# Kernel tuning notes

Hardware: AMD Instinct MI355X
Metric: run time of the kernel (lower is better)

## Reference

```python
import jax, jax.numpy as jnp
import numpy as np
import math

HEAD_DIM = 128
N_HEADS = 32
N_KV_HEADS = 8
ROPE_THETA = 10000.0


def _rotate_half(x):
    x1, x2 = jnp.split(x, 2, axis=-1)
    return jnp.concatenate([-x2, x1], axis=-1)


def _rope_cos_sin(position_ids, head_dim, theta):
    # position_ids: [B, S] int
    inv_freq = 1.0 / (theta ** (jnp.arange(0, head_dim, 2, dtype=jnp.float32) / head_dim))
    freqs = position_ids.astype(jnp.float32)[..., None] * inv_freq[None, None, :]  # [B,S,D/2]
    emb = jnp.concatenate([freqs, freqs], axis=-1)  # [B,S,D]
    return jnp.cos(emb), jnp.sin(emb)


def setup_inputs() -> dict:
    key = jax.random.key(0)
    k1, k2, k3, k4, k5 = jax.random.split(key, 5)
    B, S, H = 1, 2048, 4096
    hidden_states = jax.random.normal(k1, (B, S, H), dtype=jnp.float32)
    Wq = jax.random.normal(k2, (N_HEADS * HEAD_DIM, H), dtype=jnp.float32) * (1.0 / math.sqrt(H))
    Wk = jax.random.normal(k3, (N_KV_HEADS * HEAD_DIM, H), dtype=jnp.float32) * (1.0 / math.sqrt(H))
    Wv = jax.random.normal(k4, (N_KV_HEADS * HEAD_DIM, H), dtype=jnp.float32) * (1.0 / math.sqrt(H))
    Wo = jax.random.normal(k5, (H, N_HEADS * HEAD_DIM), dtype=jnp.float32) * (1.0 / math.sqrt(H))
    position_ids = jnp.arange(S, dtype=jnp.int32)[None, :]
    return {"hidden_states": hidden_states, "Wq": Wq, "Wk": Wk, "Wv": Wv, "Wo": Wo,
            "position_ids": position_ids}


def reference(hidden_states, Wq, Wk, Wv, Wo, position_ids):
    B, S, H = hidden_states.shape
    d = HEAD_DIM
    groups = N_HEADS // N_KV_HEADS

    # projections (torch Linear: x @ W^T)
    q = (hidden_states @ Wq.T).reshape(B, S, N_HEADS, d).transpose(0, 2, 1, 3)      # [B,Hq,S,d]
    k = (hidden_states @ Wk.T).reshape(B, S, N_KV_HEADS, d).transpose(0, 2, 1, 3)   # [B,Hk,S,d]
    v = (hidden_states @ Wv.T).reshape(B, S, N_KV_HEADS, d).transpose(0, 2, 1, 3)

    cos, sin = _rope_cos_sin(position_ids, d, ROPE_THETA)  # [B,S,d]
    cos = cos[:, None, :, :]
    sin = sin[:, None, :, :]
    q = q * cos + _rotate_half(q) * sin
    k = k * cos + _rotate_half(k) * sin

    # GQA: repeat kv heads
    k = jnp.repeat(k, groups, axis=1)  # [B,Hq,S,d]
    v = jnp.repeat(v, groups, axis=1)

    scores = jnp.einsum('bhqd,bhkd->bhqk', q, k) / math.sqrt(d)
    causal = jnp.tril(jnp.ones((S, S), dtype=bool))
    scores = jnp.where(causal[None, None], scores, jnp.finfo(jnp.float32).min)
    attn = jax.nn.softmax(scores.astype(jnp.float32), axis=-1).astype(q.dtype)

    out = jnp.einsum('bhqk,bhkd->bhqd', attn, v)        # [B,Hq,S,d]
    out = out.transpose(0, 2, 1, 3).reshape(B, S, N_HEADS * d)
    return out @ Wo.T
```

## Files before the change

### kernel.cpp

```cpp
#include <hip/hip_runtime.h>
#include <hip/hip_bf16.h>
#include <cstdint>
#include <cstddef>

#define S_LEN 2048
#define HID   4096
#define HD    128
#define NH    32
#define NKV   8
#define KVW   (NKV * HD)
#define QKVN  (HID + 2 * KVW)

typedef __bf16 bf16x8_t __attribute__((ext_vector_type(8)));
typedef float  f32x4_t  __attribute__((ext_vector_type(4)));
typedef unsigned short u16x8_t __attribute__((ext_vector_type(8)));

__device__ __forceinline__ unsigned short f2b(float f) {
  unsigned u = __float_as_uint(f);
  u += 0x7FFFu + ((u >> 16) & 1u);
  return (unsigned short)(u >> 16);
}
__device__ __forceinline__ float b2f(unsigned short v) {
  return __uint_as_float(((unsigned)v) << 16);
}
__device__ __forceinline__ void gld_lds16(const void* g, void* l) {
  __builtin_amdgcn_global_load_lds(
      (const __attribute__((address_space(1))) void*)g,
      (__attribute__((address_space(3))) void*)l, 16, 0, 0);
}

__global__ void cvt_kernel(const float* __restrict__ src,
                           unsigned short* __restrict__ dst, int n4) {
  int i = blockIdx.x * blockDim.x + threadIdx.x;
  int stride = gridDim.x * blockDim.x;
  for (; i < n4; i += stride) {
    float4 v = reinterpret_cast<const float4*>(src)[i];
    ushort4 o;
    o.x = f2b(v.x); o.y = f2b(v.y); o.z = f2b(v.z); o.w = f2b(v.w);
    reinterpret_cast<ushort4*>(dst)[i] = o;
  }
}

__global__ void rope_kernel(unsigned short* __restrict__ Q,
                            unsigned short* __restrict__ Kb,
                            const int* __restrict__ pos_ids) {
  const int total = S_LEN * (NH + NKV) * 64;
  int idx = blockIdx.x * blockDim.x + threadIdx.x;
  int stride = gridDim.x * blockDim.x;
  for (; idx < total; idx += stride) {
    int s   = idx / ((NH + NKV) * 64);
    int rem = idx % ((NH + NKV) * 64);
    int hp  = rem >> 6;
    int i   = rem & 63;
    unsigned short* ptr; int W, h;
    if (hp < NH) { ptr = Q;  W = HID; h = hp; }
    else         { ptr = Kb; W = KVW; h = hp - NH; }
    float pos = (float)pos_ids[s];
    float ang = pos * __expf(-(float)i * 0.14391156516f);
    float sn, cs;
    sincosf(ang, &sn, &cs);
    size_t base = (size_t)s * W + (size_t)h * HD + i;
    float lo = b2f(ptr[base]);
    float hi = b2f(ptr[base + 64]);
    ptr[base]      = f2b(lo * cs - hi * sn);
    ptr[base + 64] = f2b(hi * cs + lo * sn);
  }
}

template <int BN, int MODE>
__global__ __launch_bounds__(512, 4) void gemm4p_kernel(
    const unsigned short* __restrict__ A, const unsigned short* __restrict__ B,
    void* __restrict__ C0, void* __restrict__ C1, void* __restrict__ C2,
    int N, int K) {
  constexpr int NFR = BN / 64;
  constexpr int ABYTES = 128 * 128;
  constexpr int TILE_LDS = ABYTES + BN * 128;
  __shared__ char ldsB[2 * TILE_LDS];

  const int tid  = threadIdx.x;
  const int lane = tid & 63;
  const int wid  = tid >> 6;
  const int wm = wid >> 2, wn = wid & 3;
  const int lr = lane & 15, g = lane >> 4;
  const int bm = blockIdx.y * 128;
  const int bn = blockIdx.x * BN;
  const int nk = K >> 6;
  const int ni = nk >> 1;
  const int xr = (lr & 7) << 4;

  auto stage_u = [&](int t, int u) {
    if (t >= nk) return;
    const int riu = tid >> 3;
    const int cbs = ((tid & 7) << 4) ^ ((riu & 7) << 4);
    const char* src;
    if (u < 2)
      src = (const char*)A + ((size_t)(bm + u * 64 + riu) * K + t * 64) * 2 + cbs;
    else
      src = (const char*)B + ((size_t)(bn + (u - 2) * 64 + riu) * K + t * 64) * 2 + cbs;
    gld_lds16(src, ldsB + (t & 1) * TILE_LDS + u * 8192 + tid * 16);
  };

  auto rdA = [&](const char* bb, int m, int k) {
    const int row = wm * 64 + m * 16 + lr;
    return *(const bf16x8_t*)(bb + row * 128 + ((k * 64 + g * 16) ^ xr));
  };
  auto rdB = [&](const char* bb, int n, int k) {
    const int row = wn * (BN / 4) + n * 16 + lr;
    return *(const bf16x8_t*)(bb + ABYTES + row * 128 + ((k * 64 + g * 16) ^ xr));
  };

  for (int t = 0; t < 2; ++t)
    for (int u = 0; u < 2 + NFR; ++u) stage_u(t, u);
  asm volatile("s_waitcnt vmcnt(0)" ::: "memory");
  __builtin_amdgcn_sched_barrier(0);
  __builtin_amdgcn_s_barrier();

  f32x4_t acc[4][NFR];
#pragma unroll
  for (int m = 0; m < 4; ++m)
#pragma unroll
    for (int n = 0; n < NFR; ++n) acc[m][n] = f32x4_t{0.f, 0.f, 0.f, 0.f};

  bf16x8_t bfr[NFR][2], af[2][2];

#define MFMA_BLOCK(MB)                                                        \
  __builtin_amdgcn_s_setprio(1);                                              \
  _Pragma("unroll") for (int m = 0; m < 2; ++m)                               \
    _Pragma("unroll") for (int n = 0; n < NFR; ++n)                           \
      _Pragma("unroll") for (int k = 0; k < 2; ++k)                           \
        acc[(MB) + m][n] = __builtin_amdgcn_mfma_f32_16x16x32_bf16(           \
            af[m][k], bfr[n][k], acc[(MB) + m][n], 0, 0, 0);                  \
  __builtin_amdgcn_s_setprio(0);

#define GATE()                                                                \
  __builtin_amdgcn_s_barrier();                                               \
  asm volatile("s_waitcnt lgkmcnt(0)" ::: "memory");                          \
  __builtin_amdgcn_sched_barrier(0);

#define RD_A2(bb, m0)                                                         \
  _Pragma("unroll") for (int m = 0; m < 2; ++m)                               \
    _Pragma("unroll") for (int k = 0; k < 2; ++k)                             \
      af[m][k] = rdA(bb, (m0) + m, k);

#define RD_B(bb)                                                              \
  _Pragma("unroll") for (int n = 0; n < NFR; ++n)                             \
    _Pragma("unroll") for (int k = 0; k < 2; ++k)                             \
      bfr[n][k] = rdB(bb, n, k);

  for (int i = 0; i < ni; ++i) {
    const char* bE = ldsB;
    const char* bO = ldsB + TILE_LDS;
    const int tO = 2 * i + 1, tE2 = 2 * i + 2, tO2 = 2 * i + 3;
    const bool last = (i == ni - 1);

    RD_B(bE);
    RD_A2(bE, 0);
    if (i > 0) { stage_u(tO, 0); stage_u(tO, 1); }
    GATE(); MFMA_BLOCK(0);
    __builtin_amdgcn_s_barrier();

    RD_A2(bE, 2);
#pragma unroll
    for (int u = 0; u < NFR; ++u) stage_u(tE2, 2 + u);
    GATE(); MFMA_BLOCK(2);
    if (last) { asm volatile("s_waitcnt vmcnt(0)" ::: "memory"); }
    else      { asm volatile("s_waitcnt vmcnt(%0)" :: "n"(NFR) : "memory"); }
    __builtin_amdgcn_sched_barrier(0);
    __builtin_amdgcn_s_barrier();

    RD_B(bO);
    RD_A2(bO, 0);
    stage_u(tE2, 0); stage_u(tE2, 1);
    GATE(); MFMA_BLOCK(0);
    __builtin_amdgcn_s_barrier();

    RD_A2(bO, 2);
#pragma unroll
    for (int u = 0; u < NFR; ++u) stage_u(tO2, 2 + u);
    GATE(); MFMA_BLOCK(2);
    if (!last) { asm volatile("s_waitcnt vmcnt(%0)" :: "n"(NFR) : "memory"); }
    __builtin_amdgcn_sched_barrier(0);
    __builtin_amdgcn_s_barrier();
  }
#undef MFMA_BLOCK
#undef GATE
#undef RD_A2
#undef RD_B

#pragma unroll
  for (int mf = 0; mf < 4; ++mf) {
    const int row0 = bm + wm * 64 + mf * 16 + g * 4;
#pragma unroll
    for (int nf = 0; nf < NFR; ++nf) {
      const int col = bn + wn * (BN / 4) + nf * 16 + lr;
      if constexpr (MODE == 1) {
#pragma unroll
        for (int r = 0; r < 4; ++r)
          ((float*)C0)[(size_t)(row0 + r) * N + col] = acc[mf][nf][r];
      } else {
        if (col < HID) {
#pragma unroll
          for (int r = 0; r < 4; ++r)
            ((unsigned short*)C0)[(size_t)(row0 + r) * HID + col] = f2b(acc[mf][nf][r]);
        } else if (col < HID + KVW) {
#pragma unroll
          for (int r = 0; r < 4; ++r)
            ((unsigned short*)C1)[(size_t)(row0 + r) * KVW + (col - HID)] = f2b(acc[mf][nf][r]);
        } else {
          const int c2 = col - HID - KVW;
          ushort4 w;
          w.x = f2b(acc[mf][nf][0]); w.y = f2b(acc[mf][nf][1]);
          w.z = f2b(acc[mf][nf][2]); w.w = f2b(acc[mf][nf][3]);
          *(ushort4*)(void*)&((unsigned short*)C2)[(size_t)c2 * S_LEN + row0] = w;
        }
      }
    }
  }
}

__global__ __launch_bounds__(256) void attn_kernel(
    const unsigned short* __restrict__ Q, const unsigned short* __restrict__ K,
    const unsigned short* __restrict__ VtG, unsigned short* __restrict__ O) {
  __shared__ char KlB[2][16384];
  __shared__ char VtB2[2][16384];
  __shared__ unsigned short Pl[4][16][72];

  const int tid  = threadIdx.x;
  const int lane = tid & 63;
  const int wave = tid >> 6;
  const int h    = blockIdx.y;
  const int kvh  = h >> 2;
  const int pair = blockIdx.x;
  const int lr   = lane & 15;
  const int g    = lane >> 4;
  const int lk8  = g * 8;
  const float scale = 0.08838834764831845f;

  auto stageK = [&](int kv0, int buf) {
#pragma unroll
    for (int j = 0; j < 4; ++j) {
      const int row  = j * 16 + (tid >> 4);
      const int colb = ((tid & 15) << 4) ^ ((row & 15) << 4);
      const char* src =
          (const char*)(K + (size_t)(kv0 + row) * KVW + (size_t)kvh * HD) + colb;
      gld_lds16(src, &KlB[buf][row * 256 + ((tid & 15) << 4)]);
    }
  };
  auto stageV = [&](int kv0, int buf) {
#pragma unroll
    for (int j = 0; j < 4; ++j) {
      const int row  = j * 32 + (tid >> 3);
      const int colb = ((tid & 7) << 4) ^ ((row & 7) << 4);
      const char* src =
          (const char*)(VtG + ((size_t)kvh * HD + row) * S_LEN + kv0) + colb;
      gld_lds16(src, &VtB2[buf][row * 128 + ((tid & 7) << 4)]);
    }
  };
  auto rdK = [&](int buf, int n, int c) {
    const int row = n * 16 + lr;
    return *(const bf16x8_t*)&KlB[buf][row * 256 +
                                       ((c * 64 + g * 16) ^ ((lr & 15) << 4))];
  };
  auto rdV = [&](int buf, int c, int half) {
    const int row = c * 16 + lr;
    return *(const bf16x8_t*)&VtB2[buf][row * 128 +
                                        ((half * 64 + g * 16) ^ ((lr & 7) << 4))];
  };

  for (int pass = 0; pass < 2; ++pass) {
    const int qb = pass == 0 ? (31 - pair) : pair;
    const int q0 = qb * 64;
    const int qrow = q0 + wave * 16;
    const int nkv = qb + 1;

    bf16x8_t qf[4];
    {
      const unsigned short* qp = Q + (size_t)(qrow + lr) * HID + (size_t)h * HD;
#pragma unroll
      for (int c = 0; c < 4; ++c)
        qf[c] = *(const bf16x8_t*)(const void*)(qp + c * 32 + lk8);
    }
    f32x4_t oacc[8];
#pragma unroll
    for (int c = 0; c < 8; ++c) oacc[c] = f32x4_t{0.f, 0.f, 0.f, 0.f};
    float m_run = -3e38f, l_run = 0.f;

    stageK(0, 0); stageV(0, 0);
    asm volatile("s_waitcnt vmcnt(0)" ::: "memory");
    __builtin_amdgcn_sched_barrier(0);
    __builtin_amdgcn_s_barrier();

    for (int it = 0; it < nkv; ++it) {
      const int kv0 = it * 64;
      const int buf = it & 1;
      if (it + 1 < nkv) { stageK(kv0 + 64, buf ^ 1); stageV(kv0 + 64, buf ^ 1); }

      f32x4_t sacc[4];
#pragma unroll
      for (int n = 0; n < 4; ++n) sacc[n] = f32x4_t{0.f, 0.f, 0.f, 0.f};
#pragma unroll
      for (int c = 0; c < 4; ++c) {
        bf16x8_t qc = qf[c];
#pragma unroll
        for (int n = 0; n < 4; ++n)
          sacc[n] = __builtin_amdgcn_mfma_f32_16x16x32_bf16(rdK(buf, n, c), qc,
                                                            sacc[n], 0, 0, 0);
      }

      const int qg = qrow + lr;
      const bool diag = (it == nkv - 1);
      float p[16];
      float mloc = -3e38f;
#pragma unroll
      for (int n = 0; n < 4; ++n)
#pragma unroll
        for (int r = 0; r < 4; ++r) {
          float x = sacc[n][r] * scale;
          if (diag) {
            int kg = kv0 + n * 16 + g * 4 + r;
            if (kg > qg) x = -3e38f;
          }
          p[n * 4 + r] = x;
          mloc = fmaxf(mloc, x);
        }
      mloc = fmaxf(mloc, __shfl_xor(mloc, 16));
      mloc = fmaxf(mloc, __shfl_xor(mloc, 32));

      if (__any(mloc > m_run + 8.f)) {
        float m_new = fmaxf(m_run, mloc);
        float alpha = __expf(m_run - m_new);
        float a4[4];
#pragma unroll
        for (int r = 0; r < 4; ++r) a4[r] = __shfl(alpha, g * 4 + r);
#pragma unroll
        for (int c = 0; c < 8; ++c)
#pragma unroll
          for (int r = 0; r < 4; ++r) oacc[c][r] *= a4[r];
        l_run *= alpha;
        m_run = m_new;
      }

      float ssum = 0.f;
#pragma unroll
      for (int i = 0; i < 16; ++i) {
        float e = __expf(p[i] - m_run);
        p[i] = e;
        ssum += e;
      }
      ssum += __shfl_xor(ssum, 16);
      ssum += __shfl_xor(ssum, 32);
      l_run += ssum;

#pragma unroll
      for (int n = 0; n < 4; ++n) {
        ushort4 w;
        w.x = f2b(p[n * 4 + 0]); w.y = f2b(p[n * 4 + 1]);
        w.z = f2b(p[n * 4 + 2]); w.w = f2b(p[n * 4 + 3]);
        *(ushort4*)(void*)&Pl[wave][lr][n * 16 + g * 4] = w;
      }

#pragma unroll
      for (int half = 0; half < 2; ++half) {
        bf16x8_t pf = *(const bf16x8_t*)(const void*)&Pl[wave][lr][half * 32 + lk8];
#pragma unroll
        for (int c = 0; c < 8; ++c)
          oacc[c] = __builtin_amdgcn_mfma_f32_16x16x32_bf16(pf, rdV(buf, c, half),
                                                            oacc[c], 0, 0, 0);
      }

      if (it + 1 < nkv) { asm volatile("s_waitcnt vmcnt(0)" ::: "memory"); }
      __builtin_amdgcn_sched_barrier(0);
      __builtin_amdgcn_s_barrier();
    }

    float linv[4];
#pragma unroll
    for (int r = 0; r < 4; ++r) linv[r] = 1.f / __shfl(l_run, g * 4 + r);
#pragma unroll
    for (int r = 0; r < 4; ++r) {
      int row = qrow + g * 4 + r;
#pragma unroll
      for (int c = 0; c < 8; ++c)
        O[(size_t)row * HID + (size_t)h * HD + c * 16 + lr] = f2b(oacc[c][r] * linv[r]);
    }
  }
}

extern "C" void kernel_launch(void* const* d_in, const int* in_sizes, int n_in,
                              void* d_out, int out_size, void* d_ws, size_t ws_size,
                              hipStream_t stream) {
  (void)in_sizes; (void)n_in; (void)out_size; (void)ws_size;
  const float* X  = (const float*)d_in[0];
  const float* Wq = (const float*)d_in[1];
  const float* Wk = (const float*)d_in[2];
  const float* Wv = (const float*)d_in[3];
  const float* Wo = (const float*)d_in[4];
  const int*  pos = (const int*)d_in[5];
  float* out = (float*)d_out;

  unsigned short* Xb  = (unsigned short*)d_ws;
  unsigned short* Wqb = Xb  + (size_t)S_LEN * HID;
  unsigned short* Wkb = Wqb + (size_t)HID * HID;
  unsigned short* Wvb = Wkb + (size_t)KVW * HID;
  unsigned short* Wob = Wvb + (size_t)KVW * HID;
  unsigned short* Qb  = Wob + (size_t)HID * HID;
  unsigned short* Kb  = Qb  + (size_t)S_LEN * HID;
  unsigned short* VtB = Kb  + (size_t)S_LEN * KVW;
  unsigned short* AOb = VtB + (size_t)S_LEN * KVW;

  auto cvt = [&](const float* s, unsigned short* d, size_t n) {
    int n4 = (int)(n / 4);
    int grid = (n4 + 255) / 256;
    if (grid > 4096) grid = 4096;
    cvt_kernel<<<grid, 256, 0, stream>>>(s, d, n4);
  };
  cvt(X,  Xb,  (size_t)S_LEN * HID);
  cvt(Wq, Wqb, (size_t)HID * HID);
  cvt(Wk, Wkb, (size_t)KVW * HID);
  cvt(Wv, Wvb, (size_t)KVW * HID);
  cvt(Wo, Wob, (size_t)HID * HID);

  gemm4p_kernel<192, 2><<<dim3(QKVN / 192, S_LEN / 128), 512, 0, stream>>>(
      Xb, Wqb, Qb, Kb, VtB, QKVN, HID);

  rope_kernel<<<2048, 256, 0, stream>>>(Qb, Kb, pos);

  attn_kernel<<<dim3(16, NH), 256, 0, stream>>>(Qb, Kb, VtB, AOb);

  gemm4p_kernel<128, 1><<<dim3(HID / 128, S_LEN / 128), 512, 0, stream>>>(
      AOb, Wob, out, nullptr, nullptr, HID, HID);
}
```

Measured before the change: 293.2 us.

## Fold Wo bf16 conversion into attention and use 4-wave GEMM tiles

```diff
diff --git a/kernel.cpp b/kernel.cpp
--- a/kernel.cpp
+++ b/kernel.cpp
@@ -68,11 +68,11 @@
 }
 
 template <int BN, int MODE>
-__global__ __launch_bounds__(512, 4) void gemm4p_kernel(
+__global__ __launch_bounds__(256, 2) void gemm4w_kernel(
     const unsigned short* __restrict__ A, const unsigned short* __restrict__ B,
     void* __restrict__ C0, void* __restrict__ C1, void* __restrict__ C2,
     int N, int K) {
-  constexpr int NFR = BN / 64;
+  constexpr int NFRW = BN / 32;
   constexpr int ABYTES = 128 * 128;
   constexpr int TILE_LDS = ABYTES + BN * 128;
   __shared__ char ldsB[2 * TILE_LDS];
@@ -80,7 +80,7 @@
   const int tid  = threadIdx.x;
   const int lane = tid & 63;
   const int wid  = tid >> 6;
-  const int wm = wid >> 2, wn = wid & 3;
+  const int wm = wid >> 1, wn = wid & 1;
   const int lr = lane & 15, g = lane >> 4;
   const int bm = blockIdx.y * 128;
   const int bn = blockIdx.x * BN;
@@ -93,11 +93,11 @@
     const int riu = tid >> 3;
     const int cbs = ((tid & 7) << 4) ^ ((riu & 7) << 4);
     const char* src;
-    if (u < 2)
-      src = (const char*)A + ((size_t)(bm + u * 64 + riu) * K + t * 64) * 2 + cbs;
+    if (u < 4)
+      src = (const char*)A + ((size_t)(bm + u * 32 + riu) * K + t * 64) * 2 + cbs;
     else
-      src = (const char*)B + ((size_t)(bn + (u - 2) * 64 + riu) * K + t * 64) * 2 + cbs;
-    gld_lds16(src, ldsB + (t & 1) * TILE_LDS + u * 8192 + tid * 16);
+      src = (const char*)B + ((size_t)(bn + (u - 4) * 32 + riu) * K + t * 64) * 2 + cbs;
+    gld_lds16(src, ldsB + (t & 1) * TILE_LDS + u * 4096 + tid * 16);
   };
 
   auto rdA = [&](const char* bb, int m, int k) {
@@ -105,28 +105,28 @@
     return *(const bf16x8_t*)(bb + row * 128 + ((k * 64 + g * 16) ^ xr));
   };
   auto rdB = [&](const char* bb, int n, int k) {
-    const int row = wn * (BN / 4) + n * 16 + lr;
+    const int row = wn * (BN / 2) + n * 16 + lr;
     return *(const bf16x8_t*)(bb + ABYTES + row * 128 + ((k * 64 + g * 16) ^ xr));
   };
 
   for (int t = 0; t < 2; ++t)
-    for (int u = 0; u < 2 + NFR; ++u) stage_u(t, u);
+    for (int u = 0; u < 4 + NFRW; ++u) stage_u(t, u);
   asm volatile("s_waitcnt vmcnt(0)" ::: "memory");
   __builtin_amdgcn_sched_barrier(0);
   __builtin_amdgcn_s_barrier();
 
-  f32x4_t acc[4][NFR];
+  f32x4_t acc[4][NFRW];
 #pragma unroll
   for (int m = 0; m < 4; ++m)
 #pragma unroll
-    for (int n = 0; n < NFR; ++n) acc[m][n] = f32x4_t{0.f, 0.f, 0.f, 0.f};
-
-  bf16x8_t bfr[NFR][2], af[2][2];
+    for (int n = 0; n < NFRW; ++n) acc[m][n] = f32x4_t{0.f, 0.f, 0.f, 0.f};
+
+  bf16x8_t bfr[NFRW][2], af[2][2];
 
 #define MFMA_BLOCK(MB)                                                        \
   __builtin_amdgcn_s_setprio(1);                                              \
   _Pragma("unroll") for (int m = 0; m < 2; ++m)                               \
-    _Pragma("unroll") for (int n = 0; n < NFR; ++n)                           \
+    _Pragma("unroll") for (int n = 0; n < NFRW; ++n)                          \
       _Pragma("unroll") for (int k = 0; k < 2; ++k)                           \
         acc[(MB) + m][n] = __builtin_amdgcn_mfma_f32_16x16x32_bf16(           \
             af[m][k], bfr[n][k], acc[(MB) + m][n], 0, 0, 0);                  \
@@ -143,7 +143,7 @@
       af[m][k] = rdA(bb, (m0) + m, k);
 
 #define RD_B(bb)                                                              \
-  _Pragma("unroll") for (int n = 0; n < NFR; ++n)                             \
+  _Pragma("unroll") for (int n = 0; n < NFRW; ++n)                            \
     _Pragma("unroll") for (int k = 0; k < 2; ++k)                             \
       bfr[n][k] = rdB(bb, n, k);
 
@@ -155,30 +155,34 @@
 
     RD_B(bE);
     RD_A2(bE, 0);
-    if (i > 0) { stage_u(tO, 0); stage_u(tO, 1); }
+    if (i > 0) {
+#pragma unroll
+      for (int u = 0; u < 4; ++u) stage_u(tO, u);
+    }
     GATE(); MFMA_BLOCK(0);
     __builtin_amdgcn_s_barrier();
 
     RD_A2(bE, 2);
 #pragma unroll
-    for (int u = 0; u < NFR; ++u) stage_u(tE2, 2 + u);
+    for (int u = 0; u < NFRW; ++u) stage_u(tE2, 4 + u);
     GATE(); MFMA_BLOCK(2);
     if (last) { asm volatile("s_waitcnt vmcnt(0)" ::: "memory"); }
-    else      { asm volatile("s_waitcnt vmcnt(%0)" :: "n"(NFR) : "memory"); }
+    else      { asm volatile("s_waitcnt vmcnt(%0)" :: "n"(NFRW) : "memory"); }
     __builtin_amdgcn_sched_barrier(0);
     __builtin_amdgcn_s_barrier();
 
     RD_B(bO);
     RD_A2(bO, 0);
-    stage_u(tE2, 0); stage_u(tE2, 1);
+#pragma unroll
+    for (int u = 0; u < 4; ++u) stage_u(tE2, u);
     GATE(); MFMA_BLOCK(0);
     __builtin_amdgcn_s_barrier();
 
     RD_A2(bO, 2);
 #pragma unroll
-    for (int u = 0; u < NFR; ++u) stage_u(tO2, 2 + u);
+    for (int u = 0; u < NFRW; ++u) stage_u(tO2, 4 + u);
     GATE(); MFMA_BLOCK(2);
-    if (!last) { asm volatile("s_waitcnt vmcnt(%0)" :: "n"(NFR) : "memory"); }
+    if (!last) { asm volatile("s_waitcnt vmcnt(%0)" :: "n"(NFRW) : "memory"); }
     __builtin_amdgcn_sched_barrier(0);
     __builtin_amdgcn_s_barrier();
   }
@@ -191,8 +195,8 @@
   for (int mf = 0; mf < 4; ++mf) {
     const int row0 = bm + wm * 64 + mf * 16 + g * 4;
 #pragma unroll
-    for (int nf = 0; nf < NFR; ++nf) {
-      const int col = bn + wn * (BN / 4) + nf * 16 + lr;
+    for (int nf = 0; nf < NFRW; ++nf) {
+      const int col = bn + wn * (BN / 2) + nf * 16 + lr;
       if constexpr (MODE == 1) {
 #pragma unroll
         for (int r = 0; r < 4; ++r)
@@ -220,7 +224,8 @@
 
 __global__ __launch_bounds__(256) void attn_kernel(
     const unsigned short* __restrict__ Q, const unsigned short* __restrict__ K,
-    const unsigned short* __restrict__ VtG, unsigned short* __restrict__ O) {
+    const unsigned short* __restrict__ VtG, unsigned short* __restrict__ O,
+    const float* __restrict__ WoF, unsigned short* __restrict__ WoB) {
   __shared__ char KlB[2][16384];
   __shared__ char VtB2[2][16384];
   __shared__ unsigned short Pl[4][16][72];
@@ -235,6 +240,11 @@
   const int g    = lane >> 4;
   const int lk8  = g * 8;
   const float scale = 0.08838834764831845f;
+  const int blkl = h * 16 + pair;
+  const int CVT_LIM = (HID * HID) / 4;
+  int itg = 0;
+  int pendidx = 0x7FFFFFFF;
+  float4 pend;
 
   auto stageK = [&](int kv0, int buf) {
 #pragma unroll
@@ -293,6 +303,18 @@
     for (int it = 0; it < nkv; ++it) {
       const int kv0 = it * 64;
       const int buf = it & 1;
+
+      if (pendidx < CVT_LIM) {
+        ushort4 o;
+        o.x = f2b(pend.x); o.y = f2b(pend.y);
+        o.z = f2b(pend.z); o.w = f2b(pend.w);
+        reinterpret_cast<ushort4*>(WoB)[pendidx] = o;
+      }
+      pendidx = (blkl * 33 + itg) * 256 + tid;
+      ++itg;
+      if (pendidx < CVT_LIM)
+        pend = reinterpret_cast<const float4*>(WoF)[pendidx];
+
       if (it + 1 < nkv) { stageK(kv0 + 64, buf ^ 1); stageV(kv0 + 64, buf ^ 1); }
 
       f32x4_t sacc[4];
@@ -384,6 +406,13 @@
         O[(size_t)row * HID + (size_t)h * HD + c * 16 + lr] = f2b(oacc[c][r] * linv[r]);
     }
   }
+
+  if (pendidx < CVT_LIM) {
+    ushort4 o;
+    o.x = f2b(pend.x); o.y = f2b(pend.y);
+    o.z = f2b(pend.z); o.w = f2b(pend.w);
+    reinterpret_cast<ushort4*>(WoB)[pendidx] = o;
+  }
 }
 
 extern "C" void kernel_launch(void* const* d_in, const int* in_sizes, int n_in,
@@ -418,15 +447,14 @@
   cvt(Wq, Wqb, (size_t)HID * HID);
   cvt(Wk, Wkb, (size_t)KVW * HID);
   cvt(Wv, Wvb, (size_t)KVW * HID);
-  cvt(Wo, Wob, (size_t)HID * HID);
-
-  gemm4p_kernel<192, 2><<<dim3(QKVN / 192, S_LEN / 128), 512, 0, stream>>>(
+
+  gemm4w_kernel<192, 2><<<dim3(QKVN / 192, S_LEN / 128), 256, 0, stream>>>(
       Xb, Wqb, Qb, Kb, VtB, QKVN, HID);
 
   rope_kernel<<<2048, 256, 0, stream>>>(Qb, Kb, pos);
 
-  attn_kernel<<<dim3(16, NH), 256, 0, stream>>>(Qb, Kb, VtB, AOb);
-
-  gemm4p_kernel<128, 1><<<dim3(HID / 128, S_LEN / 128), 512, 0, stream>>>(
+  attn_kernel<<<dim3(16, NH), 256, 0, stream>>>(Qb, Kb, VtB, AOb, Wo, Wob);
+
+  gemm4w_kernel<128, 1><<<dim3(HID / 128, S_LEN / 128), 256, 0, stream>>>(
       AOb, Wob, out, nullptr, nullptr, HID, HID);
 }
```

New measurement: 283.0 us. 3.5% less time.
